# Kernel tuning notes

Hardware: AMD Instinct MI355X
Metric: run time of the kernel (lower is better)

The kernel has to match this reference:

```python
import jax, jax.numpy as jnp
import numpy as np

EPS = 1e-8

def _cdist(a, b):
    # Euclidean pairwise distances, torch.cdist(p=2) equivalent.
    sq = (jnp.sum(a * a, axis=1)[:, None] + jnp.sum(b * b, axis=1)[None, :]
          - 2.0 * (a @ b.T))
    return jnp.sqrt(jnp.maximum(sq, 1e-12))

def setup_inputs() -> dict:
    key = jax.random.key(0)
    k1, k2, k3, k4, k5, k6 = jax.random.split(key, 6)
    ns, n_cls, n_feat, K = 4096, 500, 256, 400
    return {
        "src_x": jax.random.normal(k1, (ns, n_feat), dtype=jnp.float32),
        "tgt_x": jax.random.normal(k2, (ns, n_feat), dtype=jnp.float32),
        "src_y": jax.random.uniform(k3, (ns, n_cls), dtype=jnp.float32),
        "tgt_y": jax.random.uniform(k4, (ns, n_cls), dtype=jnp.float32),
        "queue": jax.random.normal(k5, (n_cls, n_feat, K), dtype=jnp.float32),
        "queue_size": jax.random.randint(k6, (n_cls,), 0, K, dtype=jnp.int32),
    }

def reference(src_x, tgt_x, src_y, tgt_y, queue, queue_size):
    n_cls, n_feat, K = queue.shape
    num = queue_size.astype(queue.dtype)[:, None]                      # (C,1)
    # src_centroid: masked mean over the first queue_size[c] columns
    valid = (jnp.arange(K)[None, :] < queue_size[:, None]).astype(queue.dtype)  # (C,K)
    centroid = jnp.einsum('cfk,ck->cf', queue, valid) / jnp.maximum(num, 1.0)
    centroid = jnp.where(num > 0, centroid, 0.0)                       # (C,F)

    batch_src = src_y.T @ src_x                                        # (C,F)
    total_num = num + jnp.sum(src_y, axis=0)[:, None] + EPS            # (C,1)
    mean_src = (centroid * num + batch_src) / total_num                # (C,F)

    batch_prob = jnp.sum(tgt_y, axis=0)[:, None] + EPS                 # (C,1)
    mean_tgt = (tgt_y.T @ tgt_x) / batch_prob                          # (C,F)

    intra = jnp.diagonal(_cdist(mean_src, mean_tgt)).mean()
    inter = _cdist(mean_src, mean_src).mean()
    return intra, inter
```

## Files before the change

kernel.cpp:

```cpp
#include <hip/hip_runtime.h>
#include <math.h>

#define NS 4096
#define NC 500
#define NF 256
#define NK 400
#define KC_GEMM 16
#define KC_CS   32

#define NB_GEMM (32 * KC_GEMM * 2)
#define NB_CS   (KC_CS * 2)
#define NB_OTH  (NB_GEMM + NB_CS)
#define NB_QUE  ((NC * NF) / 32)

__global__ __launch_bounds__(256) void k_heavy(
    const float* __restrict__ Xs, const float* __restrict__ Ys, float* __restrict__ Ps,
    const float* __restrict__ Xt, const float* __restrict__ Yt, float* __restrict__ Pt,
    float* __restrict__ CSs, float* __restrict__ CSt,
    const float* __restrict__ queue, const int* __restrict__ qsize,
    float* __restrict__ qsum) {
  __shared__ float ytile[NS / KC_GEMM][16];
  const int bid = blockIdx.x;

  if (bid < NB_GEMM) {
    const int z   = bid >> 9;
    const int rem = bid & 511;
    const int kc  = rem >> 5;
    const int c0  = (rem & 31) * 16;
    const float* X = z ? Xt : Xs;
    const float* Y = z ? Yt : Ys;
    float*       P = z ? Pt : Ps;
    const int n0   = kc * (NS / KC_GEMM);
    const int cmax = (NC - c0 < 16) ? (NC - c0) : 16;

    for (int i = threadIdx.x; i < (NS / KC_GEMM) * 16; i += 256) {
      int rr = i >> 4, cc = i & 15;
      ytile[rr][cc] = (cc < cmax) ? Y[(size_t)(n0 + rr) * NC + c0 + cc] : 0.f;
    }
    __syncthreads();

    const int f = threadIdx.x;
    float acc[16];
    #pragma unroll
    for (int j = 0; j < 16; ++j) acc[j] = 0.f;

    #pragma unroll 4
    for (int n = 0; n < NS / KC_GEMM; ++n) {
      float xv = X[(size_t)(n0 + n) * NF + f];
      #pragma unroll
      for (int j = 0; j < 16; ++j) acc[j] = fmaf(ytile[n][j], xv, acc[j]);
    }
    #pragma unroll
    for (int j = 0; j < 16; ++j)
      if (c0 + j < NC) P[((size_t)kc * NC + c0 + j) * NF + f] = acc[j];

  } else if (bid < NB_OTH) {
    const int b = bid - NB_GEMM;
    const float* Y = (b >> 5) ? Yt : Ys;
    float*      CS = (b >> 5) ? CSt : CSs;
    const int kc = b & 31;
    const int n0 = kc * (NS / KC_CS);
    const int t  = threadIdx.x;
    float s0 = 0.f, s1 = 0.f;
    for (int n = n0; n < n0 + NS / KC_CS; ++n) {
      const float* row = Y + (size_t)n * NC;
      s0 += row[t];
      if (t + 256 < NC) s1 += row[t + 256];
    }
    CS[kc * 512 + t] = s0;
    if (t + 256 < NC) CS[kc * 512 + t + 256] = s1;

  } else {
    const int qb   = bid - NB_OTH;
    const int widx = threadIdx.x >> 6;
    const int lane = threadIdx.x & 63;
    const int r0   = (qb * 4 + widx) * 8;
    const int c    = r0 >> 8;
    const int qs   = qsize[c];
    const int L    = (qs + 3) >> 2;
    const float* base = queue + (size_t)r0 * NK;
    float s0 = 0.f, s1 = 0.f, s2 = 0.f, s3 = 0.f;
    float s4 = 0.f, s5 = 0.f, s6 = 0.f, s7 = 0.f;

    if (lane < L) {
      const int k = 4 * lane;
      float4 v0 = *reinterpret_cast<const float4*>(base + 0 * NK + k);
      float4 v1 = *reinterpret_cast<const float4*>(base + 1 * NK + k);
      float4 v2 = *reinterpret_cast<const float4*>(base + 2 * NK + k);
      float4 v3 = *reinterpret_cast<const float4*>(base + 3 * NK + k);
      float4 v4 = *reinterpret_cast<const float4*>(base + 4 * NK + k);
      float4 v5 = *reinterpret_cast<const float4*>(base + 5 * NK + k);
      float4 v6 = *reinterpret_cast<const float4*>(base + 6 * NK + k);
      float4 v7 = *reinterpret_cast<const float4*>(base + 7 * NK + k);
      s0 += v0.x; s1 += v1.x; s2 += v2.x; s3 += v3.x;
      s4 += v4.x; s5 += v5.x; s6 += v6.x; s7 += v7.x;
      if (k + 1 < qs) { s0 += v0.y; s1 += v1.y; s2 += v2.y; s3 += v3.y;
                        s4 += v4.y; s5 += v5.y; s6 += v6.y; s7 += v7.y; }
      if (k + 2 < qs) { s0 += v0.z; s1 += v1.z; s2 += v2.z; s3 += v3.z;
                        s4 += v4.z; s5 += v5.z; s6 += v6.z; s7 += v7.z; }
      if (k + 3 < qs) { s0 += v0.w; s1 += v1.w; s2 += v2.w; s3 += v3.w;
                        s4 += v4.w; s5 += v5.w; s6 += v6.w; s7 += v7.w; }
    }
    if (lane + 64 < L) {
      const int k = 256 + 4 * lane;
      float4 v0 = *reinterpret_cast<const float4*>(base + 0 * NK + k);
      float4 v1 = *reinterpret_cast<const float4*>(base + 1 * NK + k);
      float4 v2 = *reinterpret_cast<const float4*>(base + 2 * NK + k);
      float4 v3 = *reinterpret_cast<const float4*>(base + 3 * NK + k);
      float4 v4 = *reinterpret_cast<const float4*>(base + 4 * NK + k);
      float4 v5 = *reinterpret_cast<const float4*>(base + 5 * NK + k);
      float4 v6 = *reinterpret_cast<const float4*>(base + 6 * NK + k);
      float4 v7 = *reinterpret_cast<const float4*>(base + 7 * NK + k);
      s0 += v0.x; s1 += v1.x; s2 += v2.x; s3 += v3.x;
      s4 += v4.x; s5 += v5.x; s6 += v6.x; s7 += v7.x;
      if (k + 1 < qs) { s0 += v0.y; s1 += v1.y; s2 += v2.y; s3 += v3.y;
                        s4 += v4.y; s5 += v5.y; s6 += v6.y; s7 += v7.y; }
      if (k + 2 < qs) { s0 += v0.z; s1 += v1.z; s2 += v2.z; s3 += v3.z;
                        s4 += v4.z; s5 += v5.z; s6 += v6.z; s7 += v7.z; }
      if (k + 3 < qs) { s0 += v0.w; s1 += v1.w; s2 += v2.w; s3 += v3.w;
                        s4 += v4.w; s5 += v5.w; s6 += v6.w; s7 += v7.w; }
    }
    #pragma unroll
    for (int m = 32; m; m >>= 1) {
      s0 += __shfl_xor(s0, m); s1 += __shfl_xor(s1, m);
      s2 += __shfl_xor(s2, m); s3 += __shfl_xor(s3, m);
      s4 += __shfl_xor(s4, m); s5 += __shfl_xor(s5, m);
      s6 += __shfl_xor(s6, m); s7 += __shfl_xor(s7, m);
    }
    if (lane == 0) {
      *reinterpret_cast<float4*>(&qsum[r0])     = make_float4(s0, s1, s2, s3);
      *reinterpret_cast<float4*>(&qsum[r0 + 4]) = make_float4(s4, s5, s6, s7);
    }
  }
}

__global__ __launch_bounds__(256) void k_means(
    const float* __restrict__ qsum, const int* __restrict__ qsize,
    const float* __restrict__ Psrc, const float* __restrict__ Ptgt,
    const float* __restrict__ CSsrc, const float* __restrict__ CStgt,
    float* __restrict__ MS, float* __restrict__ MT, float* __restrict__ ipart) {
  const int c = blockIdx.x * 4 + (threadIdx.x >> 6);
  const int lane = threadIdx.x & 63;
  const int f4 = lane * 4;
  if (c >= NC) return;

  float cs_s = 0.f, cs_t = 0.f;
  #pragma unroll
  for (int kc = 0; kc < KC_CS; ++kc) {
    cs_s += CSsrc[kc * 512 + c];
    cs_t += CStgt[kc * 512 + c];
  }
  float num = (float)qsize[c];
  float4 ns = *reinterpret_cast<const float4*>(&qsum[(size_t)c * NF + f4]);
  float4 nt = make_float4(0.f, 0.f, 0.f, 0.f);
  #pragma unroll
  for (int kc = 0; kc < KC_GEMM; ++kc) {
    float4 ps = *reinterpret_cast<const float4*>(&Psrc[((size_t)kc * NC + c) * NF + f4]);
    float4 pt = *reinterpret_cast<const float4*>(&Ptgt[((size_t)kc * NC + c) * NF + f4]);
    ns.x += ps.x; ns.y += ps.y; ns.z += ps.z; ns.w += ps.w;
    nt.x += pt.x; nt.y += pt.y; nt.z += pt.z; nt.w += pt.w;
  }
  float rs = 1.f / (num + cs_s + 1e-8f);
  float rt = 1.f / (cs_t + 1e-8f);
  float4 ms = make_float4(ns.x * rs, ns.y * rs, ns.z * rs, ns.w * rs);
  float4 mt = make_float4(nt.x * rt, nt.y * rt, nt.z * rt, nt.w * rt);
  *reinterpret_cast<float4*>(&MS[(size_t)c * NF + f4]) = ms;
  *reinterpret_cast<float4*>(&MT[(size_t)c * NF + f4]) = mt;

  float dx = ms.x - mt.x, dy = ms.y - mt.y, dz = ms.z - mt.z, dw = ms.w - mt.w;
  float s = dx * dx + dy * dy + dz * dz + dw * dw;
  #pragma unroll
  for (int m = 32; m; m >>= 1) s += __shfl_xor(s, m);
  if (lane == 0) ipart[c] = sqrtf(fmaxf(s, 1e-12f));
}

#define TC 16
#define NBT 32
__global__ __launch_bounds__(256) void k_dist(const float* __restrict__ MS,
                                              float* __restrict__ epart) {
  __shared__ float a[TC][NF + 4];
  __shared__ float b[TC][NF + 4];
  const int bi = blockIdx.x & (NBT - 1);
  const int bj = blockIdx.x >> 5;

  for (int i = threadIdx.x; i < TC * (NF / 4); i += 256) {
    int rr = i >> 6, fq = (i & 63) * 4;
    int c1 = bi * TC + rr;
    int c2 = bj * TC + rr;
    float4 va = (c1 < NC) ? *reinterpret_cast<const float4*>(&MS[(size_t)c1 * NF + fq])
                          : make_float4(0.f, 0.f, 0.f, 0.f);
    float4 vb = (c2 < NC) ? *reinterpret_cast<const float4*>(&MS[(size_t)c2 * NF + fq])
                          : make_float4(0.f, 0.f, 0.f, 0.f);
    *reinterpret_cast<float4*>(&a[rr][fq]) = va;
    *reinterpret_cast<float4*>(&b[rr][fq]) = vb;
  }
  __syncthreads();

  const int i1 = threadIdx.x >> 4, i2 = threadIdx.x & 15;
  float s = 0.f;
  #pragma unroll 8
  for (int fq = 0; fq < NF; fq += 4) {
    float4 va = *reinterpret_cast<const float4*>(&a[i1][fq]);
    float4 vb = *reinterpret_cast<const float4*>(&b[i2][fq]);
    float d0 = va.x - vb.x, d1 = va.y - vb.y, d2 = va.z - vb.z, d3 = va.w - vb.w;
    s = fmaf(d0, d0, s); s = fmaf(d1, d1, s); s = fmaf(d2, d2, s); s = fmaf(d3, d3, s);
  }
  bool valid = (bi * TC + i1 < NC) && (bj * TC + i2 < NC);
  float rr = valid ? sqrtf(fmaxf(s, 1e-12f)) : 0.f;

  #pragma unroll
  for (int m = 32; m; m >>= 1) rr += __shfl_xor(rr, m);
  __shared__ float red[4];
  int wid = threadIdx.x >> 6, lane = threadIdx.x & 63;
  if (lane == 0) red[wid] = rr;
  __syncthreads();
  if (threadIdx.x == 0) epart[blockIdx.x] = red[0] + red[1] + red[2] + red[3];
}

__global__ __launch_bounds__(1024) void k_final(const float* __restrict__ ipart,
                                                const float* __restrict__ epart,
                                                float* __restrict__ out) {
  const int t = threadIdx.x;
  float si = (t < NC) ? ipart[t] : 0.f;
  float se = epart[t];
  #pragma unroll
  for (int m = 32; m; m >>= 1) { si += __shfl_xor(si, m); se += __shfl_xor(se, m); }
  __shared__ float ri[16], re[16];
  int wid = t >> 6, lane = t & 63;
  if (lane == 0) { ri[wid] = si; re[wid] = se; }
  __syncthreads();
  if (t == 0) {
    float A = 0.f, B = 0.f;
    #pragma unroll
    for (int w = 0; w < 16; ++w) { A += ri[w]; B += re[w]; }
    out[0] = A / (float)NC;
    out[1] = B / ((float)NC * (float)NC);
  }
}

extern "C" void kernel_launch(void* const* d_in, const int* in_sizes, int n_in,
                              void* d_out, int out_size, void* d_ws, size_t ws_size,
                              hipStream_t stream) {
  const float* src_x = (const float*)d_in[0];
  const float* tgt_x = (const float*)d_in[1];
  const float* src_y = (const float*)d_in[2];
  const float* tgt_y = (const float*)d_in[3];
  const float* queue = (const float*)d_in[4];
  const int*   qsize = (const int*)d_in[5];
  float* out = (float*)d_out;

  float* ws    = (float*)d_ws;
  float* qsum  = ws;
  float* Psrc  = qsum + NC * NF;
  float* Ptgt  = Psrc + (size_t)KC_GEMM * NC * NF;
  float* CSs   = Ptgt + (size_t)KC_GEMM * NC * NF;
  float* CSt   = CSs + KC_CS * 512;
  float* MS    = CSt + KC_CS * 512;
  float* MT    = MS + NC * NF;
  float* ipart = MT + NC * NF;
  float* epart = ipart + NC;

  k_heavy<<<NB_OTH + NB_QUE, 256, 0, stream>>>(
      src_x, src_y, Psrc, tgt_x, tgt_y, Ptgt, CSs, CSt, queue, qsize, qsum);

  k_means<<<(NC + 3) / 4, 256, 0, stream>>>(qsum, qsize, Psrc, Ptgt, CSs, CSt, MS, MT, ipart);

  k_dist<<<NBT * NBT, 256, 0, stream>>>(MS, epart);

  k_final<<<1, 1024, 0, stream>>>(ipart, epart, out);
}
```

Baseline: 75.83 us.

## Co-schedule GEMM and queue-reduction waves inside hybrid blocks

Restructures k_heavy so that each of 1024 hybrid blocks runs one wavefront doing a 16-class GEMM tile and three wavefronts doing queue row reductions. The GEMM wave computes float4 per lane across 256 features and reads Y straight from global memory instead of staging a shared-memory tile. Each queue wave now handles 64 rows in a loop. The aim is to overlap the compute-bound GEMM with the bandwidth-bound queue reads on the same CUs and to cut block count and LDS use. The risks are 64 accumulator registers per lane and uncoalesced scalar Y loads.

```diff
diff --git a/kernel.cpp b/kernel.cpp
--- a/kernel.cpp
+++ b/kernel.cpp
@@ -8,10 +8,9 @@
 #define KC_GEMM 16
 #define KC_CS   32
 
-#define NB_GEMM (32 * KC_GEMM * 2)
 #define NB_CS   (KC_CS * 2)
-#define NB_OTH  (NB_GEMM + NB_CS)
-#define NB_QUE  ((NC * NF) / 32)
+#define NB_HYB  1024
+#define NQW     2000
 
 __global__ __launch_bounds__(256) void k_heavy(
     const float* __restrict__ Xs, const float* __restrict__ Ys, float* __restrict__ Ps,
@@ -19,46 +18,14 @@
     float* __restrict__ CSs, float* __restrict__ CSt,
     const float* __restrict__ queue, const int* __restrict__ qsize,
     float* __restrict__ qsum) {
-  __shared__ float ytile[NS / KC_GEMM][16];
   const int bid = blockIdx.x;
-
-  if (bid < NB_GEMM) {
-    const int z   = bid >> 9;
-    const int rem = bid & 511;
-    const int kc  = rem >> 5;
-    const int c0  = (rem & 31) * 16;
-    const float* X = z ? Xt : Xs;
-    const float* Y = z ? Yt : Ys;
-    float*       P = z ? Pt : Ps;
-    const int n0   = kc * (NS / KC_GEMM);
-    const int cmax = (NC - c0 < 16) ? (NC - c0) : 16;
-
-    for (int i = threadIdx.x; i < (NS / KC_GEMM) * 16; i += 256) {
-      int rr = i >> 4, cc = i & 15;
-      ytile[rr][cc] = (cc < cmax) ? Y[(size_t)(n0 + rr) * NC + c0 + cc] : 0.f;
-    }
-    __syncthreads();
-
-    const int f = threadIdx.x;
-    float acc[16];
-    #pragma unroll
-    for (int j = 0; j < 16; ++j) acc[j] = 0.f;
-
-    #pragma unroll 4
-    for (int n = 0; n < NS / KC_GEMM; ++n) {
-      float xv = X[(size_t)(n0 + n) * NF + f];
-      #pragma unroll
-      for (int j = 0; j < 16; ++j) acc[j] = fmaf(ytile[n][j], xv, acc[j]);
-    }
-    #pragma unroll
-    for (int j = 0; j < 16; ++j)
-      if (c0 + j < NC) P[((size_t)kc * NC + c0 + j) * NF + f] = acc[j];
-
-  } else if (bid < NB_OTH) {
-    const int b = bid - NB_GEMM;
-    const float* Y = (b >> 5) ? Yt : Ys;
-    float*      CS = (b >> 5) ? CSt : CSs;
-    const int kc = b & 31;
+  const int w    = threadIdx.x >> 6;
+  const int lane = threadIdx.x & 63;
+
+  if (bid < NB_CS) {
+    const float* Y = (bid >> 5) ? Yt : Ys;
+    float*      CS = (bid >> 5) ? CSt : CSs;
+    const int kc = bid & 31;
     const int n0 = kc * (NS / KC_CS);
     const int t  = threadIdx.x;
     float s0 = 0.f, s1 = 0.f;
@@ -69,67 +36,126 @@
     }
     CS[kc * 512 + t] = s0;
     if (t + 256 < NC) CS[kc * 512 + t + 256] = s1;
-
-  } else {
-    const int qb   = bid - NB_OTH;
-    const int widx = threadIdx.x >> 6;
-    const int lane = threadIdx.x & 63;
-    const int r0   = (qb * 4 + widx) * 8;
-    const int c    = r0 >> 8;
-    const int qs   = qsize[c];
-    const int L    = (qs + 3) >> 2;
-    const float* base = queue + (size_t)r0 * NK;
-    float s0 = 0.f, s1 = 0.f, s2 = 0.f, s3 = 0.f;
-    float s4 = 0.f, s5 = 0.f, s6 = 0.f, s7 = 0.f;
-
-    if (lane < L) {
-      const int k = 4 * lane;
-      float4 v0 = *reinterpret_cast<const float4*>(base + 0 * NK + k);
-      float4 v1 = *reinterpret_cast<const float4*>(base + 1 * NK + k);
-      float4 v2 = *reinterpret_cast<const float4*>(base + 2 * NK + k);
-      float4 v3 = *reinterpret_cast<const float4*>(base + 3 * NK + k);
-      float4 v4 = *reinterpret_cast<const float4*>(base + 4 * NK + k);
-      float4 v5 = *reinterpret_cast<const float4*>(base + 5 * NK + k);
-      float4 v6 = *reinterpret_cast<const float4*>(base + 6 * NK + k);
-      float4 v7 = *reinterpret_cast<const float4*>(base + 7 * NK + k);
-      s0 += v0.x; s1 += v1.x; s2 += v2.x; s3 += v3.x;
-      s4 += v4.x; s5 += v5.x; s6 += v6.x; s7 += v7.x;
-      if (k + 1 < qs) { s0 += v0.y; s1 += v1.y; s2 += v2.y; s3 += v3.y;
-                        s4 += v4.y; s5 += v5.y; s6 += v6.y; s7 += v7.y; }
-      if (k + 2 < qs) { s0 += v0.z; s1 += v1.z; s2 += v2.z; s3 += v3.z;
-                        s4 += v4.z; s5 += v5.z; s6 += v6.z; s7 += v7.z; }
-      if (k + 3 < qs) { s0 += v0.w; s1 += v1.w; s2 += v2.w; s3 += v3.w;
-                        s4 += v4.w; s5 += v5.w; s6 += v6.w; s7 += v7.w; }
-    }
-    if (lane + 64 < L) {
-      const int k = 256 + 4 * lane;
-      float4 v0 = *reinterpret_cast<const float4*>(base + 0 * NK + k);
-      float4 v1 = *reinterpret_cast<const float4*>(base + 1 * NK + k);
-      float4 v2 = *reinterpret_cast<const float4*>(base + 2 * NK + k);
-      float4 v3 = *reinterpret_cast<const float4*>(base + 3 * NK + k);
-      float4 v4 = *reinterpret_cast<const float4*>(base + 4 * NK + k);
-      float4 v5 = *reinterpret_cast<const float4*>(base + 5 * NK + k);
-      float4 v6 = *reinterpret_cast<const float4*>(base + 6 * NK + k);
-      float4 v7 = *reinterpret_cast<const float4*>(base + 7 * NK + k);
-      s0 += v0.x; s1 += v1.x; s2 += v2.x; s3 += v3.x;
-      s4 += v4.x; s5 += v5.x; s6 += v6.x; s7 += v7.x;
-      if (k + 1 < qs) { s0 += v0.y; s1 += v1.y; s2 += v2.y; s3 += v3.y;
-                        s4 += v4.y; s5 += v5.y; s6 += v6.y; s7 += v7.y; }
-      if (k + 2 < qs) { s0 += v0.z; s1 += v1.z; s2 += v2.z; s3 += v3.z;
-                        s4 += v4.z; s5 += v5.z; s6 += v6.z; s7 += v7.z; }
-      if (k + 3 < qs) { s0 += v0.w; s1 += v1.w; s2 += v2.w; s3 += v3.w;
-                        s4 += v4.w; s5 += v5.w; s6 += v6.w; s7 += v7.w; }
+    return;
+  }
+
+  const int hb = bid - NB_CS;
+
+  if (w == (hb & 3)) {
+    const int z  = hb >> 9;
+    const int kc = (hb & 511) >> 5;
+    const int ct = hb & 31;
+    const float* X = z ? Xt : Xs;
+    const float* Y = z ? Yt : Ys;
+    float*       P = z ? Pt : Ps;
+    const int c0 = ct * 16;
+    const int n0 = kc * (NS / KC_GEMM);
+    const int f4 = lane * 4;
+    const int cmax = (NC - c0 < 16) ? (NC - c0) : 16;
+
+    float4 acc[16];
+    #pragma unroll
+    for (int j = 0; j < 16; ++j) acc[j] = make_float4(0.f, 0.f, 0.f, 0.f);
+
+    const float* Xp = X + (size_t)n0 * NF + f4;
+    const float* Yp = Y + (size_t)n0 * NC + c0;
+
+    if (cmax == 16) {
+      #pragma unroll 2
+      for (int n = 0; n < NS / KC_GEMM; ++n) {
+        float4 xv = *reinterpret_cast<const float4*>(Xp + (size_t)n * NF);
+        #pragma unroll
+        for (int j = 0; j < 16; ++j) {
+          float yv = Yp[(size_t)n * NC + j];
+          acc[j].x = fmaf(yv, xv.x, acc[j].x);
+          acc[j].y = fmaf(yv, xv.y, acc[j].y);
+          acc[j].z = fmaf(yv, xv.z, acc[j].z);
+          acc[j].w = fmaf(yv, xv.w, acc[j].w);
+        }
+      }
+    } else {
+      #pragma unroll 2
+      for (int n = 0; n < NS / KC_GEMM; ++n) {
+        float4 xv = *reinterpret_cast<const float4*>(Xp + (size_t)n * NF);
+        #pragma unroll
+        for (int j = 0; j < 4; ++j) {
+          float yv = Yp[(size_t)n * NC + j];
+          acc[j].x = fmaf(yv, xv.x, acc[j].x);
+          acc[j].y = fmaf(yv, xv.y, acc[j].y);
+          acc[j].z = fmaf(yv, xv.z, acc[j].z);
+          acc[j].w = fmaf(yv, xv.w, acc[j].w);
+        }
+      }
     }
     #pragma unroll
-    for (int m = 32; m; m >>= 1) {
-      s0 += __shfl_xor(s0, m); s1 += __shfl_xor(s1, m);
-      s2 += __shfl_xor(s2, m); s3 += __shfl_xor(s3, m);
-      s4 += __shfl_xor(s4, m); s5 += __shfl_xor(s5, m);
-      s6 += __shfl_xor(s6, m); s7 += __shfl_xor(s7, m);
-    }
-    if (lane == 0) {
-      *reinterpret_cast<float4*>(&qsum[r0])     = make_float4(s0, s1, s2, s3);
-      *reinterpret_cast<float4*>(&qsum[r0 + 4]) = make_float4(s4, s5, s6, s7);
+    for (int j = 0; j < 16; ++j)
+      if (j < cmax)
+        *reinterpret_cast<float4*>(&P[((size_t)kc * NC + c0 + j) * NF + f4]) = acc[j];
+
+  } else {
+    const int qw = w - (w > (hb & 3) ? 1 : 0);
+    const int q  = hb * 3 + qw;
+    if (q >= NQW) return;
+    const int r0 = q * 64;
+    const int c  = r0 >> 8;
+    const int qs = qsize[c];
+    const int L  = (qs + 3) >> 2;
+
+    for (int ch = 0; ch < 8; ++ch) {
+      const int rb = r0 + ch * 8;
+      const float* base = queue + (size_t)rb * NK;
+      float s0 = 0.f, s1 = 0.f, s2 = 0.f, s3 = 0.f;
+      float s4 = 0.f, s5 = 0.f, s6 = 0.f, s7 = 0.f;
+
+      if (lane < L) {
+        const int k = 4 * lane;
+        float4 v0 = *reinterpret_cast<const float4*>(base + 0 * NK + k);
+        float4 v1 = *reinterpret_cast<const float4*>(base + 1 * NK + k);
+        float4 v2 = *reinterpret_cast<const float4*>(base + 2 * NK + k);
+        float4 v3 = *reinterpret_cast<const float4*>(base + 3 * NK + k);
+        float4 v4 = *reinterpret_cast<const float4*>(base + 4 * NK + k);
+        float4 v5 = *reinterpret_cast<const float4*>(base + 5 * NK + k);
+        float4 v6 = *reinterpret_cast<const float4*>(base + 6 * NK + k);
+        float4 v7 = *reinterpret_cast<const float4*>(base + 7 * NK + k);
+        s0 += v0.x; s1 += v1.x; s2 += v2.x; s3 += v3.x;
+        s4 += v4.x; s5 += v5.x; s6 += v6.x; s7 += v7.x;
+        if (k + 1 < qs) { s0 += v0.y; s1 += v1.y; s2 += v2.y; s3 += v3.y;
+                          s4 += v4.y; s5 += v5.y; s6 += v6.y; s7 += v7.y; }
+        if (k + 2 < qs) { s0 += v0.z; s1 += v1.z; s2 += v2.z; s3 += v3.z;
+                          s4 += v4.z; s5 += v5.z; s6 += v6.z; s7 += v7.z; }
+        if (k + 3 < qs) { s0 += v0.w; s1 += v1.w; s2 += v2.w; s3 += v3.w;
+                          s4 += v4.w; s5 += v5.w; s6 += v6.w; s7 += v7.w; }
+      }
+      if (lane + 64 < L) {
+        const int k = 256 + 4 * lane;
+        float4 v0 = *reinterpret_cast<const float4*>(base + 0 * NK + k);
+        float4 v1 = *reinterpret_cast<const float4*>(base + 1 * NK + k);
+        float4 v2 = *reinterpret_cast<const float4*>(base + 2 * NK + k);
+        float4 v3 = *reinterpret_cast<const float4*>(base + 3 * NK + k);
+        float4 v4 = *reinterpret_cast<const float4*>(base + 4 * NK + k);
+        float4 v5 = *reinterpret_cast<const float4*>(base + 5 * NK + k);
+        float4 v6 = *reinterpret_cast<const float4*>(base + 6 * NK + k);
+        float4 v7 = *reinterpret_cast<const float4*>(base + 7 * NK + k);
+        s0 += v0.x; s1 += v1.x; s2 += v2.x; s3 += v3.x;
+        s4 += v4.x; s5 += v5.x; s6 += v6.x; s7 += v7.x;
+        if (k + 1 < qs) { s0 += v0.y; s1 += v1.y; s2 += v2.y; s3 += v3.y;
+                          s4 += v4.y; s5 += v5.y; s6 += v6.y; s7 += v7.y; }
+        if (k + 2 < qs) { s0 += v0.z; s1 += v1.z; s2 += v2.z; s3 += v3.z;
+                          s4 += v4.z; s5 += v5.z; s6 += v6.z; s7 += v7.z; }
+        if (k + 3 < qs) { s0 += v0.w; s1 += v1.w; s2 += v2.w; s3 += v3.w;
+                          s4 += v4.w; s5 += v5.w; s6 += v6.w; s7 += v7.w; }
+      }
+      #pragma unroll
+      for (int m = 32; m; m >>= 1) {
+        s0 += __shfl_xor(s0, m); s1 += __shfl_xor(s1, m);
+        s2 += __shfl_xor(s2, m); s3 += __shfl_xor(s3, m);
+        s4 += __shfl_xor(s4, m); s5 += __shfl_xor(s5, m);
+        s6 += __shfl_xor(s6, m); s7 += __shfl_xor(s7, m);
+      }
+      if (lane == 0) {
+        *reinterpret_cast<float4*>(&qsum[rb])     = make_float4(s0, s1, s2, s3);
+        *reinterpret_cast<float4*>(&qsum[rb + 4]) = make_float4(s4, s5, s6, s7);
+      }
     }
   }
 }
@@ -232,7 +258,7 @@
   if (t == 0) {
     float A = 0.f, B = 0.f;
     #pragma unroll
-    for (int w = 0; w < 16; ++w) { A += ri[w]; B += re[w]; }
+    for (int w2 = 0; w2 < 16; ++w2) { A += ri[w2]; B += re[w2]; }
     out[0] = A / (float)NC;
     out[1] = B / ((float)NC * (float)NC);
   }
@@ -260,7 +286,7 @@
   float* ipart = MT + NC * NF;
   float* epart = ipart + NC;
 
-  k_heavy<<<NB_OTH + NB_QUE, 256, 0, stream>>>(
+  k_heavy<<<NB_CS + NB_HYB, 256, 0, stream>>>(
       src_x, src_y, Psrc, tgt_x, tgt_y, Ptgt, CSs, CSt, queue, qsize, qsum);
 
   k_means<<<(NC + 3) / 4, 256, 0, stream>>>(qsum, qsize, Psrc, Ptgt, CSs, CSt, MS, MT, ipart);
```

Measured after the change: 96.50 us. 1.27x slower.

## Fuse queue reduction and column sums into GEMM blocks with software pipelining

Applied to the files above, without the earlier changes.

Merges the three block roles of k_heavy into a single uniform 1024-block grid. Each GEMM block interleaves queue-segment loads with 32-row GEMM chunks, so the queue reduction's memory traffic overlaps the FMA work. It also computes the Y column sums from the already-staged shared tile, which removes the separate column-sum blocks. The changes add vectorized LDS reads and a launch-bounds occupancy hint, at the cost of more register pressure and a serialized dependency chain per block.

```diff
diff --git a/kernel.cpp b/kernel.cpp
--- a/kernel.cpp
+++ b/kernel.cpp
@@ -6,120 +6,71 @@
 #define NF 256
 #define NK 400
 #define KC_GEMM 16
-#define KC_CS   32
-
-#define NB_GEMM (32 * KC_GEMM * 2)
-#define NB_CS   (KC_CS * 2)
-#define NB_OTH  (NB_GEMM + NB_CS)
-#define NB_QUE  ((NC * NF) / 32)
-
-__global__ __launch_bounds__(256) void k_heavy(
+#define NQJ 16000
+
+__global__ __launch_bounds__(256, 4) void k_heavy(
     const float* __restrict__ Xs, const float* __restrict__ Ys, float* __restrict__ Ps,
     const float* __restrict__ Xt, const float* __restrict__ Yt, float* __restrict__ Pt,
     float* __restrict__ CSs, float* __restrict__ CSt,
     const float* __restrict__ queue, const int* __restrict__ qsize,
     float* __restrict__ qsum) {
-  __shared__ float ytile[NS / KC_GEMM][16];
-  const int bid = blockIdx.x;
-
-  if (bid < NB_GEMM) {
-    const int z   = bid >> 9;
-    const int rem = bid & 511;
-    const int kc  = rem >> 5;
-    const int c0  = (rem & 31) * 16;
-    const float* X = z ? Xt : Xs;
-    const float* Y = z ? Yt : Ys;
-    float*       P = z ? Pt : Ps;
-    const int n0   = kc * (NS / KC_GEMM);
-    const int cmax = (NC - c0 < 16) ? (NC - c0) : 16;
-
-    for (int i = threadIdx.x; i < (NS / KC_GEMM) * 16; i += 256) {
-      int rr = i >> 4, cc = i & 15;
-      ytile[rr][cc] = (cc < cmax) ? Y[(size_t)(n0 + rr) * NC + c0 + cc] : 0.f;
-    }
-    __syncthreads();
-
-    const int f = threadIdx.x;
-    float acc[16];
-    #pragma unroll
-    for (int j = 0; j < 16; ++j) acc[j] = 0.f;
-
-    #pragma unroll 4
-    for (int n = 0; n < NS / KC_GEMM; ++n) {
-      float xv = X[(size_t)(n0 + n) * NF + f];
-      #pragma unroll
-      for (int j = 0; j < 16; ++j) acc[j] = fmaf(ytile[n][j], xv, acc[j]);
-    }
-    #pragma unroll
-    for (int j = 0; j < 16; ++j)
-      if (c0 + j < NC) P[((size_t)kc * NC + c0 + j) * NF + f] = acc[j];
-
-  } else if (bid < NB_OTH) {
-    const int b = bid - NB_GEMM;
-    const float* Y = (b >> 5) ? Yt : Ys;
-    float*      CS = (b >> 5) ? CSt : CSs;
-    const int kc = b & 31;
-    const int n0 = kc * (NS / KC_CS);
-    const int t  = threadIdx.x;
-    float s0 = 0.f, s1 = 0.f;
-    for (int n = n0; n < n0 + NS / KC_CS; ++n) {
-      const float* row = Y + (size_t)n * NC;
-      s0 += row[t];
-      if (t + 256 < NC) s1 += row[t + 256];
-    }
-    CS[kc * 512 + t] = s0;
-    if (t + 256 < NC) CS[kc * 512 + t + 256] = s1;
-
-  } else {
-    const int qb   = bid - NB_OTH;
-    const int widx = threadIdx.x >> 6;
-    const int lane = threadIdx.x & 63;
-    const int r0   = (qb * 4 + widx) * 8;
-    const int c    = r0 >> 8;
-    const int qs   = qsize[c];
-    const int L    = (qs + 3) >> 2;
-    const float* base = queue + (size_t)r0 * NK;
-    float s0 = 0.f, s1 = 0.f, s2 = 0.f, s3 = 0.f;
-    float s4 = 0.f, s5 = 0.f, s6 = 0.f, s7 = 0.f;
-
-    if (lane < L) {
-      const int k = 4 * lane;
-      float4 v0 = *reinterpret_cast<const float4*>(base + 0 * NK + k);
-      float4 v1 = *reinterpret_cast<const float4*>(base + 1 * NK + k);
-      float4 v2 = *reinterpret_cast<const float4*>(base + 2 * NK + k);
-      float4 v3 = *reinterpret_cast<const float4*>(base + 3 * NK + k);
-      float4 v4 = *reinterpret_cast<const float4*>(base + 4 * NK + k);
-      float4 v5 = *reinterpret_cast<const float4*>(base + 5 * NK + k);
-      float4 v6 = *reinterpret_cast<const float4*>(base + 6 * NK + k);
-      float4 v7 = *reinterpret_cast<const float4*>(base + 7 * NK + k);
-      s0 += v0.x; s1 += v1.x; s2 += v2.x; s3 += v3.x;
-      s4 += v4.x; s5 += v5.x; s6 += v6.x; s7 += v7.x;
-      if (k + 1 < qs) { s0 += v0.y; s1 += v1.y; s2 += v2.y; s3 += v3.y;
-                        s4 += v4.y; s5 += v5.y; s6 += v6.y; s7 += v7.y; }
-      if (k + 2 < qs) { s0 += v0.z; s1 += v1.z; s2 += v2.z; s3 += v3.z;
-                        s4 += v4.z; s5 += v5.z; s6 += v6.z; s7 += v7.z; }
-      if (k + 3 < qs) { s0 += v0.w; s1 += v1.w; s2 += v2.w; s3 += v3.w;
-                        s4 += v4.w; s5 += v5.w; s6 += v6.w; s7 += v7.w; }
-    }
-    if (lane + 64 < L) {
-      const int k = 256 + 4 * lane;
-      float4 v0 = *reinterpret_cast<const float4*>(base + 0 * NK + k);
-      float4 v1 = *reinterpret_cast<const float4*>(base + 1 * NK + k);
-      float4 v2 = *reinterpret_cast<const float4*>(base + 2 * NK + k);
-      float4 v3 = *reinterpret_cast<const float4*>(base + 3 * NK + k);
-      float4 v4 = *reinterpret_cast<const float4*>(base + 4 * NK + k);
-      float4 v5 = *reinterpret_cast<const float4*>(base + 5 * NK + k);
-      float4 v6 = *reinterpret_cast<const float4*>(base + 6 * NK + k);
-      float4 v7 = *reinterpret_cast<const float4*>(base + 7 * NK + k);
-      s0 += v0.x; s1 += v1.x; s2 += v2.x; s3 += v3.x;
-      s4 += v4.x; s5 += v5.x; s6 += v6.x; s7 += v7.x;
-      if (k + 1 < qs) { s0 += v0.y; s1 += v1.y; s2 += v2.y; s3 += v3.y;
-                        s4 += v4.y; s5 += v5.y; s6 += v6.y; s7 += v7.y; }
-      if (k + 2 < qs) { s0 += v0.z; s1 += v1.z; s2 += v2.z; s3 += v3.z;
-                        s4 += v4.z; s5 += v5.z; s6 += v6.z; s7 += v7.z; }
-      if (k + 3 < qs) { s0 += v0.w; s1 += v1.w; s2 += v2.w; s3 += v3.w;
-                        s4 += v4.w; s5 += v5.w; s6 += v6.w; s7 += v7.w; }
-    }
+  __shared__ float ytile[256][16];
+  const int hb   = blockIdx.x;
+  const int tid  = threadIdx.x;
+  const int w    = tid >> 6;
+  const int lane = tid & 63;
+
+  const int z  = hb >> 9;
+  const int kc = (hb >> 5) & 15;
+  const int c0 = (hb & 31) * 16;
+  const float* X = z ? Xt : Xs;
+  const float* Y = z ? Yt : Ys;
+  float*       P = z ? Pt : Ps;
+  float*      CS = z ? CSt : CSs;
+  const int n0   = kc * 256;
+  const int cmax = (NC - c0 < 16) ? (NC - c0) : 16;
+
+  float4 ld0, ld1, ld2, ld3, ld4, ld5, ld6, ld7;
+  float  s0 = 0.f, s1 = 0.f, s2 = 0.f, s3 = 0.f, s4 = 0.f, s5 = 0.f, s6 = 0.f, s7 = 0.f;
+  const int qb = hb * 16 + w * 4;
+
+  auto q_issue = [&](int q, int seg) {
+    if (q >= NQJ) return;
+    const int qs = qsize[q >> 5];
+    const int L  = (qs + 3) >> 2;
+    const int kidx = (seg << 6) + lane;
+    if (kidx < L) {
+      const float* base = queue + (size_t)(q << 3) * NK + (kidx << 2);
+      ld0 = *reinterpret_cast<const float4*>(base + 0 * NK);
+      ld1 = *reinterpret_cast<const float4*>(base + 1 * NK);
+      ld2 = *reinterpret_cast<const float4*>(base + 2 * NK);
+      ld3 = *reinterpret_cast<const float4*>(base + 3 * NK);
+      ld4 = *reinterpret_cast<const float4*>(base + 4 * NK);
+      ld5 = *reinterpret_cast<const float4*>(base + 5 * NK);
+      ld6 = *reinterpret_cast<const float4*>(base + 6 * NK);
+      ld7 = *reinterpret_cast<const float4*>(base + 7 * NK);
+    }
+  };
+  auto q_consume = [&](int q, int seg) {
+    if (q >= NQJ) return;
+    const int qs = qsize[q >> 5];
+    const int L  = (qs + 3) >> 2;
+    if (seg == 0) { s0 = s1 = s2 = s3 = s4 = s5 = s6 = s7 = 0.f; }
+    const int kidx = (seg << 6) + lane;
+    if (kidx < L) {
+      const int k = kidx << 2;
+      s0 += ld0.x; s1 += ld1.x; s2 += ld2.x; s3 += ld3.x;
+      s4 += ld4.x; s5 += ld5.x; s6 += ld6.x; s7 += ld7.x;
+      if (k + 1 < qs) { s0 += ld0.y; s1 += ld1.y; s2 += ld2.y; s3 += ld3.y;
+                        s4 += ld4.y; s5 += ld5.y; s6 += ld6.y; s7 += ld7.y; }
+      if (k + 2 < qs) { s0 += ld0.z; s1 += ld1.z; s2 += ld2.z; s3 += ld3.z;
+                        s4 += ld4.z; s5 += ld5.z; s6 += ld6.z; s7 += ld7.z; }
+      if (k + 3 < qs) { s0 += ld0.w; s1 += ld1.w; s2 += ld2.w; s3 += ld3.w;
+                        s4 += ld4.w; s5 += ld5.w; s6 += ld6.w; s7 += ld7.w; }
+    }
+  };
+  auto q_finish = [&](int q) {
+    if (q >= NQJ) return;
     #pragma unroll
     for (int m = 32; m; m >>= 1) {
       s0 += __shfl_xor(s0, m); s1 += __shfl_xor(s1, m);
@@ -128,10 +79,66 @@
       s6 += __shfl_xor(s6, m); s7 += __shfl_xor(s7, m);
     }
     if (lane == 0) {
-      *reinterpret_cast<float4*>(&qsum[r0])     = make_float4(s0, s1, s2, s3);
-      *reinterpret_cast<float4*>(&qsum[r0 + 4]) = make_float4(s4, s5, s6, s7);
-    }
-  }
+      *reinterpret_cast<float4*>(&qsum[(q << 3)])     = make_float4(s0, s1, s2, s3);
+      *reinterpret_cast<float4*>(&qsum[(q << 3) + 4]) = make_float4(s4, s5, s6, s7);
+    }
+  };
+
+  q_issue(qb + 0, 0);
+
+  for (int i = tid; i < 256 * 16; i += 256) {
+    int rr = i >> 4, cc = i & 15;
+    ytile[rr][cc] = (cc < cmax) ? Y[(size_t)(n0 + rr) * NC + c0 + cc] : 0.f;
+  }
+  __syncthreads();
+
+  float acc[16];
+  #pragma unroll
+  for (int j = 0; j < 16; ++j) acc[j] = 0.f;
+  const float* Xp = X + (size_t)n0 * NF + tid;
+
+  auto gemm_chunk = [&](int ch) {
+    const int nb = ch << 5;
+    #pragma unroll 4
+    for (int n = nb; n < nb + 32; ++n) {
+      float xv = Xp[(size_t)n * NF];
+      float4 y0 = *reinterpret_cast<const float4*>(&ytile[n][0]);
+      float4 y1 = *reinterpret_cast<const float4*>(&ytile[n][4]);
+      float4 y2 = *reinterpret_cast<const float4*>(&ytile[n][8]);
+      float4 y3 = *reinterpret_cast<const float4*>(&ytile[n][12]);
+      acc[0]  = fmaf(y0.x, xv, acc[0]);  acc[1]  = fmaf(y0.y, xv, acc[1]);
+      acc[2]  = fmaf(y0.z, xv, acc[2]);  acc[3]  = fmaf(y0.w, xv, acc[3]);
+      acc[4]  = fmaf(y1.x, xv, acc[4]);  acc[5]  = fmaf(y1.y, xv, acc[5]);
+      acc[6]  = fmaf(y1.z, xv, acc[6]);  acc[7]  = fmaf(y1.w, xv, acc[7]);
+      acc[8]  = fmaf(y2.x, xv, acc[8]);  acc[9]  = fmaf(y2.y, xv, acc[9]);
+      acc[10] = fmaf(y2.z, xv, acc[10]); acc[11] = fmaf(y2.w, xv, acc[11]);
+      acc[12] = fmaf(y3.x, xv, acc[12]); acc[13] = fmaf(y3.y, xv, acc[13]);
+      acc[14] = fmaf(y3.z, xv, acc[14]); acc[15] = fmaf(y3.w, xv, acc[15]);
+    }
+  };
+
+  gemm_chunk(0); q_consume(qb + 0, 0); q_issue(qb + 0, 1);
+  gemm_chunk(1); q_consume(qb + 0, 1); q_finish(qb + 0); q_issue(qb + 1, 0);
+  gemm_chunk(2); q_consume(qb + 1, 0); q_issue(qb + 1, 1);
+  gemm_chunk(3); q_consume(qb + 1, 1); q_finish(qb + 1); q_issue(qb + 2, 0);
+  gemm_chunk(4); q_consume(qb + 2, 0); q_issue(qb + 2, 1);
+  gemm_chunk(5); q_consume(qb + 2, 1); q_finish(qb + 2); q_issue(qb + 3, 0);
+  gemm_chunk(6); q_consume(qb + 3, 0); q_issue(qb + 3, 1);
+  gemm_chunk(7); q_consume(qb + 3, 1); q_finish(qb + 3);
+
+  #pragma unroll
+  for (int j = 0; j < 4; ++j) {
+    const int cc = w * 4 + j;
+    float t = ytile[lane][cc] + ytile[lane + 64][cc]
+            + ytile[lane + 128][cc] + ytile[lane + 192][cc];
+    #pragma unroll
+    for (int m = 32; m; m >>= 1) t += __shfl_xor(t, m);
+    if (lane == 0) CS[kc * 512 + c0 + cc] = t;
+  }
+
+  #pragma unroll
+  for (int j = 0; j < 16; ++j)
+    if (j < cmax) P[((size_t)kc * NC + c0 + j) * NF + tid] = acc[j];
 }
 
 __global__ __launch_bounds__(256) void k_means(
@@ -146,7 +153,7 @@
 
   float cs_s = 0.f, cs_t = 0.f;
   #pragma unroll
-  for (int kc = 0; kc < KC_CS; ++kc) {
+  for (int kc = 0; kc < KC_GEMM; ++kc) {
     cs_s += CSsrc[kc * 512 + c];
     cs_t += CStgt[kc * 512 + c];
   }
@@ -232,7 +239,7 @@
   if (t == 0) {
     float A = 0.f, B = 0.f;
     #pragma unroll
-    for (int w = 0; w < 16; ++w) { A += ri[w]; B += re[w]; }
+    for (int w2 = 0; w2 < 16; ++w2) { A += ri[w2]; B += re[w2]; }
     out[0] = A / (float)NC;
     out[1] = B / ((float)NC * (float)NC);
   }
@@ -254,13 +261,13 @@
   float* Psrc  = qsum + NC * NF;
   float* Ptgt  = Psrc + (size_t)KC_GEMM * NC * NF;
   float* CSs   = Ptgt + (size_t)KC_GEMM * NC * NF;
-  float* CSt   = CSs + KC_CS * 512;
-  float* MS    = CSt + KC_CS * 512;
+  float* CSt   = CSs + KC_GEMM * 512;
+  float* MS    = CSt + KC_GEMM * 512;
   float* MT    = MS + NC * NF;
   float* ipart = MT + NC * NF;
   float* epart = ipart + NC;
 
-  k_heavy<<<NB_OTH + NB_QUE, 256, 0, stream>>>(
+  k_heavy<<<1024, 256, 0, stream>>>(
       src_x, src_y, Psrc, tgt_x, tgt_y, Ptgt, CSs, CSt, queue, qsize, qsum);
 
   k_means<<<(NC + 3) / 4, 256, 0, stream>>>(qsum, qsize, Psrc, Ptgt, CSs, CSt, MS, MT, ipart);
```

After: 107.4 us. 1.42x slower.

## Persistent fused heavy kernel interleaving GEMM tiles with queue reductions, fold column sums

Applied to the files above, without the earlier changes.

The heavy kernel now runs as a fixed grid of 1024 blocks. Each block does one GEMM tile plus up to four queue-reduction chunks, and the slot of the GEMM tile is staggered by block index modulo 5 so compute-bound and bandwidth-bound work mix across CUs. The separate column-sum blocks are gone: label column sums are taken while the Y tile is staged into shared memory. Shared-memory reads of the Y tile are vectorised to float4, and launch bounds request 4 blocks per SM. The risk is less parallelism per launch and extra barriers inside the loop.

```diff
diff --git a/kernel.cpp b/kernel.cpp
--- a/kernel.cpp
+++ b/kernel.cpp
@@ -6,130 +6,140 @@
 #define NF 256
 #define NK 400
 #define KC_GEMM 16
-#define KC_CS   32
-
-#define NB_GEMM (32 * KC_GEMM * 2)
-#define NB_CS   (KC_CS * 2)
-#define NB_OTH  (NB_GEMM + NB_CS)
-#define NB_QUE  ((NC * NF) / 32)
-
-__global__ __launch_bounds__(256) void k_heavy(
+#define NQB 4000
+
+__global__ __launch_bounds__(256, 4) void k_heavy(
     const float* __restrict__ Xs, const float* __restrict__ Ys, float* __restrict__ Ps,
     const float* __restrict__ Xt, const float* __restrict__ Yt, float* __restrict__ Pt,
     float* __restrict__ CSs, float* __restrict__ CSt,
     const float* __restrict__ queue, const int* __restrict__ qsize,
     float* __restrict__ qsum) {
-  __shared__ float ytile[NS / KC_GEMM][16];
-  const int bid = blockIdx.x;
-
-  if (bid < NB_GEMM) {
-    const int z   = bid >> 9;
-    const int rem = bid & 511;
-    const int kc  = rem >> 5;
-    const int c0  = (rem & 31) * 16;
-    const float* X = z ? Xt : Xs;
-    const float* Y = z ? Yt : Ys;
-    float*       P = z ? Pt : Ps;
-    const int n0   = kc * (NS / KC_GEMM);
-    const int cmax = (NC - c0 < 16) ? (NC - c0) : 16;
-
-    for (int i = threadIdx.x; i < (NS / KC_GEMM) * 16; i += 256) {
-      int rr = i >> 4, cc = i & 15;
-      ytile[rr][cc] = (cc < cmax) ? Y[(size_t)(n0 + rr) * NC + c0 + cc] : 0.f;
-    }
-    __syncthreads();
-
-    const int f = threadIdx.x;
-    float acc[16];
-    #pragma unroll
-    for (int j = 0; j < 16; ++j) acc[j] = 0.f;
-
-    #pragma unroll 4
-    for (int n = 0; n < NS / KC_GEMM; ++n) {
-      float xv = X[(size_t)(n0 + n) * NF + f];
+  __shared__ float ytile[256][16];
+  __shared__ float csbuf[256];
+  const int b    = blockIdx.x;
+  const int tid  = threadIdx.x;
+  const int w    = tid >> 6;
+  const int lane = tid & 63;
+  const int hp   = b % 5;
+
+  for (int it = 0; it < 5; ++it) {
+    if (it == hp) {
+      const int z  = b >> 9;
+      const int kc = (b >> 5) & 15;
+      const int c0 = (b & 31) * 16;
+      const float* X = z ? Xt : Xs;
+      const float* Y = z ? Yt : Ys;
+      float*       P = z ? Pt : Ps;
+      float*      CS = z ? CSt : CSs;
+      const int n0   = kc * 256;
+      const int cmax = (NC - c0 < 16) ? (NC - c0) : 16;
+
+      float csum = 0.f;
+      for (int i = tid; i < 256 * 16; i += 256) {
+        int rr = i >> 4, cc = i & 15;
+        float v = (cc < cmax) ? Y[(size_t)(n0 + rr) * NC + c0 + cc] : 0.f;
+        ytile[rr][cc] = v;
+        csum += v;
+      }
+      csbuf[tid] = csum;
+      __syncthreads();
+
+      float acc[16];
       #pragma unroll
-      for (int j = 0; j < 16; ++j) acc[j] = fmaf(ytile[n][j], xv, acc[j]);
-    }
-    #pragma unroll
-    for (int j = 0; j < 16; ++j)
-      if (c0 + j < NC) P[((size_t)kc * NC + c0 + j) * NF + f] = acc[j];
-
-  } else if (bid < NB_OTH) {
-    const int b = bid - NB_GEMM;
-    const float* Y = (b >> 5) ? Yt : Ys;
-    float*      CS = (b >> 5) ? CSt : CSs;
-    const int kc = b & 31;
-    const int n0 = kc * (NS / KC_CS);
-    const int t  = threadIdx.x;
-    float s0 = 0.f, s1 = 0.f;
-    for (int n = n0; n < n0 + NS / KC_CS; ++n) {
-      const float* row = Y + (size_t)n * NC;
-      s0 += row[t];
-      if (t + 256 < NC) s1 += row[t + 256];
-    }
-    CS[kc * 512 + t] = s0;
-    if (t + 256 < NC) CS[kc * 512 + t + 256] = s1;
-
-  } else {
-    const int qb   = bid - NB_OTH;
-    const int widx = threadIdx.x >> 6;
-    const int lane = threadIdx.x & 63;
-    const int r0   = (qb * 4 + widx) * 8;
-    const int c    = r0 >> 8;
-    const int qs   = qsize[c];
-    const int L    = (qs + 3) >> 2;
-    const float* base = queue + (size_t)r0 * NK;
-    float s0 = 0.f, s1 = 0.f, s2 = 0.f, s3 = 0.f;
-    float s4 = 0.f, s5 = 0.f, s6 = 0.f, s7 = 0.f;
-
-    if (lane < L) {
-      const int k = 4 * lane;
-      float4 v0 = *reinterpret_cast<const float4*>(base + 0 * NK + k);
-      float4 v1 = *reinterpret_cast<const float4*>(base + 1 * NK + k);
-      float4 v2 = *reinterpret_cast<const float4*>(base + 2 * NK + k);
-      float4 v3 = *reinterpret_cast<const float4*>(base + 3 * NK + k);
-      float4 v4 = *reinterpret_cast<const float4*>(base + 4 * NK + k);
-      float4 v5 = *reinterpret_cast<const float4*>(base + 5 * NK + k);
-      float4 v6 = *reinterpret_cast<const float4*>(base + 6 * NK + k);
-      float4 v7 = *reinterpret_cast<const float4*>(base + 7 * NK + k);
-      s0 += v0.x; s1 += v1.x; s2 += v2.x; s3 += v3.x;
-      s4 += v4.x; s5 += v5.x; s6 += v6.x; s7 += v7.x;
-      if (k + 1 < qs) { s0 += v0.y; s1 += v1.y; s2 += v2.y; s3 += v3.y;
-                        s4 += v4.y; s5 += v5.y; s6 += v6.y; s7 += v7.y; }
-      if (k + 2 < qs) { s0 += v0.z; s1 += v1.z; s2 += v2.z; s3 += v3.z;
-                        s4 += v4.z; s5 += v5.z; s6 += v6.z; s7 += v7.z; }
-      if (k + 3 < qs) { s0 += v0.w; s1 += v1.w; s2 += v2.w; s3 += v3.w;
-                        s4 += v4.w; s5 += v5.w; s6 += v6.w; s7 += v7.w; }
-    }
-    if (lane + 64 < L) {
-      const int k = 256 + 4 * lane;
-      float4 v0 = *reinterpret_cast<const float4*>(base + 0 * NK + k);
-      float4 v1 = *reinterpret_cast<const float4*>(base + 1 * NK + k);
-      float4 v2 = *reinterpret_cast<const float4*>(base + 2 * NK + k);
-      float4 v3 = *reinterpret_cast<const float4*>(base + 3 * NK + k);
-      float4 v4 = *reinterpret_cast<const float4*>(base + 4 * NK + k);
-      float4 v5 = *reinterpret_cast<const float4*>(base + 5 * NK + k);
-      float4 v6 = *reinterpret_cast<const float4*>(base + 6 * NK + k);
-      float4 v7 = *reinterpret_cast<const float4*>(base + 7 * NK + k);
-      s0 += v0.x; s1 += v1.x; s2 += v2.x; s3 += v3.x;
-      s4 += v4.x; s5 += v5.x; s6 += v6.x; s7 += v7.x;
-      if (k + 1 < qs) { s0 += v0.y; s1 += v1.y; s2 += v2.y; s3 += v3.y;
-                        s4 += v4.y; s5 += v5.y; s6 += v6.y; s7 += v7.y; }
-      if (k + 2 < qs) { s0 += v0.z; s1 += v1.z; s2 += v2.z; s3 += v3.z;
-                        s4 += v4.z; s5 += v5.z; s6 += v6.z; s7 += v7.z; }
-      if (k + 3 < qs) { s0 += v0.w; s1 += v1.w; s2 += v2.w; s3 += v3.w;
-                        s4 += v4.w; s5 += v5.w; s6 += v6.w; s7 += v7.w; }
-    }
-    #pragma unroll
-    for (int m = 32; m; m >>= 1) {
-      s0 += __shfl_xor(s0, m); s1 += __shfl_xor(s1, m);
-      s2 += __shfl_xor(s2, m); s3 += __shfl_xor(s3, m);
-      s4 += __shfl_xor(s4, m); s5 += __shfl_xor(s5, m);
-      s6 += __shfl_xor(s6, m); s7 += __shfl_xor(s7, m);
-    }
-    if (lane == 0) {
-      *reinterpret_cast<float4*>(&qsum[r0])     = make_float4(s0, s1, s2, s3);
-      *reinterpret_cast<float4*>(&qsum[r0 + 4]) = make_float4(s4, s5, s6, s7);
+      for (int j = 0; j < 16; ++j) acc[j] = 0.f;
+      const float* Xp = X + (size_t)n0 * NF + tid;
+
+      #pragma unroll 4
+      for (int n = 0; n < 256; ++n) {
+        float xv = Xp[(size_t)n * NF];
+        float4 y0 = *reinterpret_cast<const float4*>(&ytile[n][0]);
+        float4 y1 = *reinterpret_cast<const float4*>(&ytile[n][4]);
+        float4 y2 = *reinterpret_cast<const float4*>(&ytile[n][8]);
+        float4 y3 = *reinterpret_cast<const float4*>(&ytile[n][12]);
+        acc[0]  = fmaf(y0.x, xv, acc[0]);  acc[1]  = fmaf(y0.y, xv, acc[1]);
+        acc[2]  = fmaf(y0.z, xv, acc[2]);  acc[3]  = fmaf(y0.w, xv, acc[3]);
+        acc[4]  = fmaf(y1.x, xv, acc[4]);  acc[5]  = fmaf(y1.y, xv, acc[5]);
+        acc[6]  = fmaf(y1.z, xv, acc[6]);  acc[7]  = fmaf(y1.w, xv, acc[7]);
+        acc[8]  = fmaf(y2.x, xv, acc[8]);  acc[9]  = fmaf(y2.y, xv, acc[9]);
+        acc[10] = fmaf(y2.z, xv, acc[10]); acc[11] = fmaf(y2.w, xv, acc[11]);
+        acc[12] = fmaf(y3.x, xv, acc[12]); acc[13] = fmaf(y3.y, xv, acc[13]);
+        acc[14] = fmaf(y3.z, xv, acc[14]); acc[15] = fmaf(y3.w, xv, acc[15]);
+      }
+
+      if (tid < 16) {
+        float t = 0.f;
+        #pragma unroll
+        for (int j = 0; j < 16; ++j) t += csbuf[tid + 16 * j];
+        CS[kc * 512 + c0 + tid] = t;
+      }
+
+      #pragma unroll
+      for (int j = 0; j < 16; ++j)
+        if (j < cmax) P[((size_t)kc * NC + c0 + j) * NF + tid] = acc[j];
+      __syncthreads();
+
+    } else {
+      const int j = it - (it > hp ? 1 : 0);
+      const int q = j * 1024 + b;
+      if (q < NQB) {
+        const int r0 = q * 32 + w * 8;
+        const int c  = r0 >> 8;
+        const int qs = qsize[c];
+        const int L  = (qs + 3) >> 2;
+        const float* base = queue + (size_t)r0 * NK;
+        float s0 = 0.f, s1 = 0.f, s2 = 0.f, s3 = 0.f;
+        float s4 = 0.f, s5 = 0.f, s6 = 0.f, s7 = 0.f;
+
+        if (lane < L) {
+          const int k = 4 * lane;
+          float4 v0 = *reinterpret_cast<const float4*>(base + 0 * NK + k);
+          float4 v1 = *reinterpret_cast<const float4*>(base + 1 * NK + k);
+          float4 v2 = *reinterpret_cast<const float4*>(base + 2 * NK + k);
+          float4 v3 = *reinterpret_cast<const float4*>(base + 3 * NK + k);
+          float4 v4 = *reinterpret_cast<const float4*>(base + 4 * NK + k);
+          float4 v5 = *reinterpret_cast<const float4*>(base + 5 * NK + k);
+          float4 v6 = *reinterpret_cast<const float4*>(base + 6 * NK + k);
+          float4 v7 = *reinterpret_cast<const float4*>(base + 7 * NK + k);
+          s0 += v0.x; s1 += v1.x; s2 += v2.x; s3 += v3.x;
+          s4 += v4.x; s5 += v5.x; s6 += v6.x; s7 += v7.x;
+          if (k + 1 < qs) { s0 += v0.y; s1 += v1.y; s2 += v2.y; s3 += v3.y;
+                            s4 += v4.y; s5 += v5.y; s6 += v6.y; s7 += v7.y; }
+          if (k + 2 < qs) { s0 += v0.z; s1 += v1.z; s2 += v2.z; s3 += v3.z;
+                            s4 += v4.z; s5 += v5.z; s6 += v6.z; s7 += v7.z; }
+          if (k + 3 < qs) { s0 += v0.w; s1 += v1.w; s2 += v2.w; s3 += v3.w;
+                            s4 += v4.w; s5 += v5.w; s6 += v6.w; s7 += v7.w; }
+        }
+        if (lane + 64 < L) {
+          const int k = 256 + 4 * lane;
+          float4 v0 = *reinterpret_cast<const float4*>(base + 0 * NK + k);
+          float4 v1 = *reinterpret_cast<const float4*>(base + 1 * NK + k);
+          float4 v2 = *reinterpret_cast<const float4*>(base + 2 * NK + k);
+          float4 v3 = *reinterpret_cast<const float4*>(base + 3 * NK + k);
+          float4 v4 = *reinterpret_cast<const float4*>(base + 4 * NK + k);
+          float4 v5 = *reinterpret_cast<const float4*>(base + 5 * NK + k);
+          float4 v6 = *reinterpret_cast<const float4*>(base + 6 * NK + k);
+          float4 v7 = *reinterpret_cast<const float4*>(base + 7 * NK + k);
+          s0 += v0.x; s1 += v1.x; s2 += v2.x; s3 += v3.x;
+          s4 += v4.x; s5 += v5.x; s6 += v6.x; s7 += v7.x;
+          if (k + 1 < qs) { s0 += v0.y; s1 += v1.y; s2 += v2.y; s3 += v3.y;
+                            s4 += v4.y; s5 += v5.y; s6 += v6.y; s7 += v7.y; }
+          if (k + 2 < qs) { s0 += v0.z; s1 += v1.z; s2 += v2.z; s3 += v3.z;
+                            s4 += v4.z; s5 += v5.z; s6 += v6.z; s7 += v7.z; }
+          if (k + 3 < qs) { s0 += v0.w; s1 += v1.w; s2 += v2.w; s3 += v3.w;
+                            s4 += v4.w; s5 += v5.w; s6 += v6.w; s7 += v7.w; }
+        }
+        #pragma unroll
+        for (int m = 32; m; m >>= 1) {
+          s0 += __shfl_xor(s0, m); s1 += __shfl_xor(s1, m);
+          s2 += __shfl_xor(s2, m); s3 += __shfl_xor(s3, m);
+          s4 += __shfl_xor(s4, m); s5 += __shfl_xor(s5, m);
+          s6 += __shfl_xor(s6, m); s7 += __shfl_xor(s7, m);
+        }
+        if (lane == 0) {
+          *reinterpret_cast<float4*>(&qsum[r0])     = make_float4(s0, s1, s2, s3);
+          *reinterpret_cast<float4*>(&qsum[r0 + 4]) = make_float4(s4, s5, s6, s7);
+        }
+      }
     }
   }
 }
@@ -146,7 +156,7 @@
 
   float cs_s = 0.f, cs_t = 0.f;
   #pragma unroll
-  for (int kc = 0; kc < KC_CS; ++kc) {
+  for (int kc = 0; kc < KC_GEMM; ++kc) {
     cs_s += CSsrc[kc * 512 + c];
     cs_t += CStgt[kc * 512 + c];
   }
@@ -232,7 +242,7 @@
   if (t == 0) {
     float A = 0.f, B = 0.f;
     #pragma unroll
-    for (int w = 0; w < 16; ++w) { A += ri[w]; B += re[w]; }
+    for (int w2 = 0; w2 < 16; ++w2) { A += ri[w2]; B += re[w2]; }
     out[0] = A / (float)NC;
     out[1] = B / ((float)NC * (float)NC);
   }
@@ -254,13 +264,13 @@
   float* Psrc  = qsum + NC * NF;
   float* Ptgt  = Psrc + (size_t)KC_GEMM * NC * NF;
   float* CSs   = Ptgt + (size_t)KC_GEMM * NC * NF;
-  float* CSt   = CSs + KC_CS * 512;
-  float* MS    = CSt + KC_CS * 512;
+  float* CSt   = CSs + KC_GEMM * 512;
+  float* MS    = CSt + KC_GEMM * 512;
   float* MT    = MS + NC * NF;
   float* ipart = MT + NC * NF;
   float* epart = ipart + NC;
 
-  k_heavy<<<NB_OTH + NB_QUE, 256, 0, stream>>>(
+  k_heavy<<<1024, 256, 0, stream>>>(
       src_x, src_y, Psrc, tgt_x, tgt_y, Ptgt, CSs, CSt, queue, qsize, qsum);
 
   k_means<<<(NC + 3) / 4, 256, 0, stream>>>(qsum, qsize, Psrc, Ptgt, CSs, CSt, MS, MT, ipart);
```

After: 83.53 us. 10.2% more time.
